# Kernel tuning notes

Measured on AMD Instinct MI355X. Metric: run time of the kernel, lower is better.

## Reference

```python
import jax, jax.numpy as jnp
import numpy as np

B, M, N, DQ, H = 4, 4096, 4096, 256, 64

def setup_inputs() -> dict:
    key = jax.random.key(0)
    k1, k2, k3, k4 = jax.random.split(key, 4)
    x = jax.random.normal(k1, (B, M, DQ), dtype=jnp.float32)
    cond = jax.random.normal(k2, (B, N, DQ), dtype=jnp.float32)
    Wq = jax.random.normal(k3, (DQ, H), dtype=jnp.float32) * (1.0 / np.sqrt(DQ))
    Wkv = jax.random.normal(k4, (DQ, 2 * H), dtype=jnp.float32) * (1.0 / np.sqrt(DQ))
    return {"x": x, "cond": cond, "Wq": Wq, "Wkv": Wkv}

def reference(x, cond, Wq, Wkv):
    h = Wq.shape[1]
    q = jnp.einsum('bmi,ih->bmh', x, Wq)          # [B,M,H]
    kv = jnp.einsum('bni,ih->bnh', cond, Wkv)     # [B,N,2H]
    k, v = jnp.split(kv, 2, axis=-1)              # each [B,N,H]
    qk = jnp.einsum('bmd,bnd->bmn', q, k) / jnp.sqrt(jnp.asarray(h, q.dtype))
    attn = jax.nn.softmax(qk, axis=-1)            # [B,M,N]
    out = jnp.einsum('bmn,bnd->bmd', attn, v)     # [B,M,H]
    return out
```

## Files before the change

kernel.cpp:

```cpp
#include <hip/hip_runtime.h>
#include <hip/hip_bf16.h>
#include <cstdint>


#define BB 4
#define MM 4096
#define NN 4096
#define DQm 256
#define DH 64
#define NSP 8
#define NITER (NN / 64 / NSP)
#define QSCALE 0.18033688011112042f

typedef _Float16 half8 __attribute__((ext_vector_type(8)));
typedef _Float16 half4 __attribute__((ext_vector_type(4)));
typedef float floatx16 __attribute__((ext_vector_type(16)));

static __device__ __forceinline__ unsigned pkrtz(float a, float b) {
    union { __fp16 h __attribute__((ext_vector_type(2))); unsigned u; } cv;
    cv.h = __builtin_amdgcn_cvt_pkrtz(a, b);
    return cv.u;
}

__global__ __launch_bounds__(256) void wtrans_kernel(const float* __restrict__ Wq,
                                                     const float* __restrict__ Wkv,
                                                     _Float16* __restrict__ wt) {
    int cout = blockIdx.x;
    int t = threadIdx.x;
    float v = (cout < 64) ? Wq[t * 64 + cout] * QSCALE : Wkv[t * 128 + (cout - 64)];
    _Float16 hi = (_Float16)v;
    _Float16 lo = (_Float16)(v - (float)hi);
    wt[cout * DQm + t] = hi;
    wt[192 * DQm + cout * DQm + t] = lo;
}

__global__ __launch_bounds__(256) void proj_kernel(const float* __restrict__ x,
                                                   const float* __restrict__ cond,
                                                   const _Float16* __restrict__ wt,
                                                   _Float16* __restrict__ q_h,
                                                   _Float16* __restrict__ k_h,
                                                   _Float16* __restrict__ vt_h) {
    __shared__ __align__(16) _Float16 xh[64][264];
    __shared__ __align__(16) _Float16 xl[64][264];
    const int t = threadIdx.x;
    const bool isq = blockIdx.x < (BB * MM / 64);
    const int blk = isq ? blockIdx.x : blockIdx.x - BB * MM / 64;
    const long row0 = (long)blk * 64;
    const float4* xg = (const float4*)((isq ? x : cond) + row0 * DQm);
#pragma unroll
    for (int it = 0; it < 16; ++it) {
        int fid = t + it * 256;
        int row = fid >> 6, c4 = fid & 63;
        float4 v = xg[fid];
        half4 hh = {(_Float16)v.x, (_Float16)v.y, (_Float16)v.z, (_Float16)v.w};
        half4 hl = {(_Float16)(v.x - (float)hh[0]), (_Float16)(v.y - (float)hh[1]),
                    (_Float16)(v.z - (float)hh[2]), (_Float16)(v.w - (float)hh[3])};
        *(half4*)(&xh[row][c4 * 4]) = hh;
        *(half4*)(&xl[row][c4 * 4]) = hl;
    }
    __syncthreads();
    const int lane = t & 63, w = t >> 6, c = lane & 31, h = lane >> 5;
    const _Float16* wlo = wt + 192 * DQm;

    if (isq) {
        const int rt = w & 1, ct = w >> 1;
        floatx16 a1, a2, a3;
#pragma unroll
        for (int i = 0; i < 16; ++i) { a1[i] = 0.f; a2[i] = 0.f; a3[i] = 0.f; }
#pragma unroll
        for (int kt = 0; kt < 16; ++kt) {
            half8 ah = *(const half8*)(&xh[rt * 32 + c][kt * 16 + h * 8]);
            half8 al = *(const half8*)(&xl[rt * 32 + c][kt * 16 + h * 8]);
            half8 bh = *(const half8*)(wt  + (long)(ct * 32 + c) * DQm + kt * 16 + h * 8);
            half8 bl = *(const half8*)(wlo + (long)(ct * 32 + c) * DQm + kt * 16 + h * 8);
            a1 = __builtin_amdgcn_mfma_f32_32x32x16_f16(ah, bh, a1, 0, 0, 0);
            a2 = __builtin_amdgcn_mfma_f32_32x32x16_f16(ah, bl, a2, 0, 0, 0);
            a3 = __builtin_amdgcn_mfma_f32_32x32x16_f16(al, bh, a3, 0, 0, 0);
        }
#pragma unroll
        for (int r = 0; r < 16; ++r) {
            int m = (r & 3) + 8 * (r >> 2) + 4 * h;
            q_h[(row0 + rt * 32 + m) * DH + ct * 32 + c] = (_Float16)(a1[r] + a2[r] + a3[r]);
        }
    } else {
        const int rt = w & 1, ctp = w >> 1;
        floatx16 a1[2], a2[2], a3[2];
#pragma unroll
        for (int i = 0; i < 16; ++i) {
            a1[0][i] = 0.f; a2[0][i] = 0.f; a3[0][i] = 0.f;
            a1[1][i] = 0.f; a2[1][i] = 0.f; a3[1][i] = 0.f;
        }
#pragma unroll
        for (int kt = 0; kt < 16; ++kt) {
            half8 ah = *(const half8*)(&xh[rt * 32 + c][kt * 16 + h * 8]);
            half8 al = *(const half8*)(&xl[rt * 32 + c][kt * 16 + h * 8]);
#pragma unroll
            for (int i = 0; i < 2; ++i) {
                long wrow = 64 + (ctp * 2 + i) * 32 + c;
                half8 bh = *(const half8*)(wt  + wrow * DQm + kt * 16 + h * 8);
                half8 bl = *(const half8*)(wlo + wrow * DQm + kt * 16 + h * 8);
                a1[i] = __builtin_amdgcn_mfma_f32_32x32x16_f16(ah, bh, a1[i], 0, 0, 0);
                a2[i] = __builtin_amdgcn_mfma_f32_32x32x16_f16(ah, bl, a2[i], 0, 0, 0);
                a3[i] = __builtin_amdgcn_mfma_f32_32x32x16_f16(al, bh, a3[i], 0, 0, 0);
            }
        }
#pragma unroll
        for (int i = 0; i < 2; ++i) {
            int cout = (ctp * 2 + i) * 32 + c;
            if (cout < 64) {
#pragma unroll
                for (int r = 0; r < 16; ++r) {
                    int m = (r & 3) + 8 * (r >> 2) + 4 * h;
                    k_h[(row0 + rt * 32 + m) * DH + cout] =
                        (_Float16)(a1[i][r] + a2[i][r] + a3[i][r]);
                }
            } else {
                int d = cout - 64;
                long bb = row0 >> 12;
#pragma unroll
                for (int s2 = 0; s2 < 4; ++s2) {
                    long n = row0 + rt * 32 + 8 * s2 + 4 * h;
                    half4 hv;
#pragma unroll
                    for (int j = 0; j < 4; ++j)
                        hv[j] = (_Float16)(a1[i][s2 * 4 + j] + a2[i][s2 * 4 + j] +
                                           a3[i][s2 * 4 + j]);
                    *(half4*)(vt_h + (bb * DH + d) * NN + (n & 4095)) = hv;
                }
            }
        }
    }
}

__global__ __launch_bounds__(256, 4) void fa_kernel(const _Float16* __restrict__ q_h,
                                                    const _Float16* __restrict__ k_h,
                                                    const _Float16* __restrict__ vt_h,
                                                    float* __restrict__ Opart,
                                                    float2* __restrict__ ml) {
    __shared__ __align__(16) _Float16 k_lds[64][72];
    __shared__ __align__(16) _Float16 vt_lds[64][72];

    const int t = threadIdx.x;
    const int w = t >> 6;
    const int lane = t & 63;
    const int c = lane & 31;
    const int h = lane >> 5;

    const int bid = blockIdx.x;
    const int sp = bid >> 7;
    const int b  = (bid >> 5) & 3;
    const int mt = bid & 31;
    const int mbase = mt * 128 + w * 32;
    const long qrow = (long)b * MM + mbase + c;

    half8 qf[4];
#pragma unroll
    for (int kt = 0; kt < 4; ++kt)
        qf[kt] = *(const half8*)(q_h + qrow * DH + kt * 16 + h * 8);

    floatx16 Oc0, Oc1;
#pragma unroll
    for (int i = 0; i < 16; ++i) { Oc0[i] = 0.f; Oc1[i] = 0.f; }
    float m_run = -INFINITY, l_run = 0.f;

#pragma unroll 1
    for (int nt = sp * NITER; nt < sp * NITER + NITER; ++nt) {
        const int n0 = nt * 64;
        __syncthreads();
        {
            const uint4* kg = (const uint4*)(k_h + ((long)b * NN + n0) * DH);
#pragma unroll
            for (int it = 0; it < 2; ++it) {
                int cid = t + it * 256;
                int r = cid >> 3, q = cid & 7;
                *(uint4*)(&k_lds[r][q * 8]) = kg[cid];
                *(uint4*)(&vt_lds[r][q * 8]) =
                    *(const uint4*)(vt_h + ((long)b * DH + r) * NN + n0 + q * 8);
            }
        }
        __syncthreads();

        floatx16 Sc[2];
#pragma unroll
        for (int a = 0; a < 2; ++a) {
            floatx16 acc;
#pragma unroll
            for (int i = 0; i < 16; ++i) acc[i] = 0.f;
#pragma unroll
            for (int kt = 0; kt < 4; ++kt) {
                half8 af = *(const half8*)(&k_lds[a * 32 + c][kt * 16 + h * 8]);
                acc = __builtin_amdgcn_mfma_f32_32x32x16_f16(af, qf[kt], acc, 0, 0, 0);
            }
            Sc[a] = acc;
        }

        float tmax = -INFINITY;
#pragma unroll
        for (int a = 0; a < 2; ++a)
#pragma unroll
            for (int r = 0; r < 16; ++r) tmax = fmaxf(tmax, Sc[a][r]);
        tmax = fmaxf(tmax, __shfl_xor(tmax, 32, 64));
        if (__any(tmax > m_run + 8.0f)) {
            float m_new = fmaxf(m_run, tmax);
            float alpha = exp2f(m_run - m_new);
            l_run *= alpha;
#pragma unroll
            for (int i = 0; i < 16; ++i) { Oc0[i] *= alpha; Oc1[i] *= alpha; }
            m_run = m_new;
        }
        float tsum = 0.f;
#pragma unroll
        for (int a = 0; a < 2; ++a)
#pragma unroll
            for (int r = 0; r < 16; ++r) {
                float p = exp2f(Sc[a][r] - m_run);
                Sc[a][r] = p;
                tsum += p;
            }
        tsum += __shfl_xor(tsum, 32, 64);
        l_run += tsum;

#pragma unroll
        for (int a = 0; a < 2; ++a) {
            uint2 pk0 = {pkrtz(Sc[a][0],  Sc[a][1]),  pkrtz(Sc[a][2],  Sc[a][3])};
            uint2 pk1 = {pkrtz(Sc[a][4],  Sc[a][5]),  pkrtz(Sc[a][6],  Sc[a][7])};
            uint2 pk2 = {pkrtz(Sc[a][8],  Sc[a][9]),  pkrtz(Sc[a][10], Sc[a][11])};
            uint2 pk3 = {pkrtz(Sc[a][12], Sc[a][13]), pkrtz(Sc[a][14], Sc[a][15])};
            union { uint4 u; half8 f; } f0, f1;
#if __has_builtin(__builtin_amdgcn_permlane32_swap)
            {
                auto r0 = __builtin_amdgcn_permlane32_swap(pk0.x, pk1.x, false, false);
                auto r1 = __builtin_amdgcn_permlane32_swap(pk0.y, pk1.y, false, false);
                auto r2 = __builtin_amdgcn_permlane32_swap(pk2.x, pk3.x, false, false);
                auto r3 = __builtin_amdgcn_permlane32_swap(pk2.y, pk3.y, false, false);
                f0.u.x = r0[0]; f0.u.z = r0[1];
                f0.u.y = r1[0]; f0.u.w = r1[1];
                f1.u.x = r2[0]; f1.u.z = r2[1];
                f1.u.y = r3[0]; f1.u.w = r3[1];
            }
#else
            {
                uint2 s0, s1, ex0, ex1;
                s0.x = h ? pk0.x : pk1.x;  s0.y = h ? pk0.y : pk1.y;
                s1.x = h ? pk2.x : pk3.x;  s1.y = h ? pk2.y : pk3.y;
                ex0.x = __shfl_xor((int)s0.x, 32, 64);
                ex0.y = __shfl_xor((int)s0.y, 32, 64);
                ex1.x = __shfl_xor((int)s1.x, 32, 64);
                ex1.y = __shfl_xor((int)s1.y, 32, 64);
                f0.u.x = h ? ex0.x : pk0.x;  f0.u.y = h ? ex0.y : pk0.y;
                f0.u.z = h ? pk1.x : ex0.x;  f0.u.w = h ? pk1.y : ex0.y;
                f1.u.x = h ? ex1.x : pk2.x;  f1.u.y = h ? ex1.y : pk2.y;
                f1.u.z = h ? pk3.x : ex1.x;  f1.u.w = h ? pk3.y : ex1.y;
            }
#endif
#pragma unroll
            for (int bq = 0; bq < 2; ++bq) {
                int kt = 2 * a + bq;
                half8 pf = bq ? f1.f : f0.f;
                half8 vf0 = *(const half8*)(&vt_lds[c][kt * 16 + h * 8]);
                half8 vf1 = *(const half8*)(&vt_lds[32 + c][kt * 16 + h * 8]);
                Oc0 = __builtin_amdgcn_mfma_f32_32x32x16_f16(vf0, pf, Oc0, 0, 0, 0);
                Oc1 = __builtin_amdgcn_mfma_f32_32x32x16_f16(vf1, pf, Oc1, 0, 0, 0);
            }
        }
    }

    const long obase = ((long)sp * BB * MM + (long)b * MM + mbase + c) * DH;
#pragma unroll
    for (int dt = 0; dt < 2; ++dt) {
        const floatx16& O = dt ? Oc1 : Oc0;
#pragma unroll
        for (int s2 = 0; s2 < 4; ++s2) {
            float4 v;
            v.x = O[s2 * 4 + 0]; v.y = O[s2 * 4 + 1];
            v.z = O[s2 * 4 + 2]; v.w = O[s2 * 4 + 3];
            *(float4*)(Opart + obase + dt * 32 + s2 * 8 + h * 4) = v;
        }
    }
    if (h == 0)
        ml[((long)sp * BB + b) * MM + mbase + c] = make_float2(m_run, l_run);
}

__global__ __launch_bounds__(256) void merge_kernel(const float* __restrict__ Opart,
                                                    const float2* __restrict__ ml,
                                                    float* __restrict__ out) {
    const long gid = (long)blockIdx.x * 256 + threadIdx.x;
    const long row = gid >> 6;
    float2 p[NSP];
    float mmax = -INFINITY;
#pragma unroll
    for (int i = 0; i < NSP; ++i) {
        p[i] = ml[(long)i * BB * MM + row];
        mmax = fmaxf(mmax, p[i].x);
    }
    float denom = 0.f, o = 0.f;
#pragma unroll
    for (int i = 0; i < NSP; ++i) {
        float ai = exp2f(p[i].x - mmax);
        denom += ai * p[i].y;
        o += ai * Opart[(long)i * BB * MM * DH + gid];
    }
    out[gid] = o / denom;
}

extern "C" void kernel_launch(void* const* d_in, const int* in_sizes, int n_in,
                              void* d_out, int out_size, void* d_ws, size_t ws_size,
                              hipStream_t stream) {
    const float* x    = (const float*)d_in[0];
    const float* cond = (const float*)d_in[1];
    const float* Wq   = (const float*)d_in[2];
    const float* Wkv  = (const float*)d_in[3];
    float* out = (float*)d_out;

    char* ws = (char*)d_ws;
    _Float16* wt   = (_Float16*)(ws);
    _Float16* q_h  = (_Float16*)(ws + 196608);
    _Float16* k_h  = (_Float16*)(ws + 196608 + 2097152);
    _Float16* vt_h = (_Float16*)(ws + 196608 + 2 * 2097152);
    float*    Op   = (float*)(ws + 196608 + 3 * 2097152);
    float2*   mlp  = (float2*)(ws + 196608 + 3 * 2097152 + (size_t)NSP * 4194304);

    wtrans_kernel<<<192, 256, 0, stream>>>(Wq, Wkv, wt);
    proj_kernel<<<BB * (MM + NN) / 64, 256, 0, stream>>>(x, cond, wt, q_h, k_h, vt_h);
    fa_kernel<<<NSP * BB * 32, 256, 0, stream>>>(q_h, k_h, vt_h, Op, mlp);
    merge_kernel<<<BB * MM * DH / 256, 256, 0, stream>>>(Op, mlp, out);
}
```

Baseline: 134.9 us.

## Add MFMA priority hints, tree reductions, fixed m_run init, vectorized merge

Wraps the QK and PV MFMA blocks in s_setprio so waves issuing matrix ops get scheduling priority over softmax ALU work. The serial row-max and row-sum chains become tree reductions to shorten dependency latency. m_run starts at 8.0 instead of -inf, which avoids a guaranteed rescale on the first tile but relies on the lazy-rescale threshold keeping exp2 values bounded. The merge kernel now handles four outputs per thread with float4 loads and stores, using a quarter as many threads and one reciprocal.

```diff
diff --git a/kernel.cpp b/kernel.cpp
--- a/kernel.cpp
+++ b/kernel.cpp
@@ -161,7 +161,7 @@
     floatx16 Oc0, Oc1;
 #pragma unroll
     for (int i = 0; i < 16; ++i) { Oc0[i] = 0.f; Oc1[i] = 0.f; }
-    float m_run = -INFINITY, l_run = 0.f;
+    float m_run = 8.0f, l_run = 0.f;
 
 #pragma unroll 1
     for (int nt = sp * NITER; nt < sp * NITER + NITER; ++nt) {
@@ -181,6 +181,7 @@
         __syncthreads();
 
         floatx16 Sc[2];
+        __builtin_amdgcn_s_setprio(1);
 #pragma unroll
         for (int a = 0; a < 2; ++a) {
             floatx16 acc;
@@ -193,12 +194,16 @@
             }
             Sc[a] = acc;
         }
-
-        float tmax = -INFINITY;
-#pragma unroll
-        for (int a = 0; a < 2; ++a)
-#pragma unroll
-            for (int r = 0; r < 16; ++r) tmax = fmaxf(tmax, Sc[a][r]);
+        __builtin_amdgcn_s_setprio(0);
+
+        float t8v[8];
+#pragma unroll
+        for (int i = 0; i < 8; ++i)
+            t8v[i] = fmaxf(fmaxf(Sc[0][2 * i], Sc[0][2 * i + 1]),
+                           fmaxf(Sc[1][2 * i], Sc[1][2 * i + 1]));
+        float ta = fmaxf(fmaxf(t8v[0], t8v[1]), t8v[2]);
+        float tb = fmaxf(fmaxf(t8v[3], t8v[4]), t8v[5]);
+        float tmax = fmaxf(fmaxf(ta, tb), fmaxf(t8v[6], t8v[7]));
         tmax = fmaxf(tmax, __shfl_xor(tmax, 32, 64));
         if (__any(tmax > m_run + 8.0f)) {
             float m_new = fmaxf(m_run, tmax);
@@ -208,17 +213,24 @@
             for (int i = 0; i < 16; ++i) { Oc0[i] *= alpha; Oc1[i] *= alpha; }
             m_run = m_new;
         }
-        float tsum = 0.f;
 #pragma unroll
         for (int a = 0; a < 2; ++a)
 #pragma unroll
-            for (int r = 0; r < 16; ++r) {
-                float p = exp2f(Sc[a][r] - m_run);
-                Sc[a][r] = p;
-                tsum += p;
-            }
-        tsum += __shfl_xor(tsum, 32, 64);
-        l_run += tsum;
+            for (int r = 0; r < 16; ++r) Sc[a][r] = exp2f(Sc[a][r] - m_run);
+
+        {
+            float ts[16];
+#pragma unroll
+            for (int i = 0; i < 16; ++i) ts[i] = Sc[0][i] + Sc[1][i];
+#pragma unroll
+            for (int i = 0; i < 8; ++i) ts[i] += ts[i + 8];
+#pragma unroll
+            for (int i = 0; i < 4; ++i) ts[i] += ts[i + 4];
+            ts[0] += ts[2]; ts[1] += ts[3];
+            float tsum = ts[0] + ts[1];
+            tsum += __shfl_xor(tsum, 32, 64);
+            l_run += tsum;
+        }
 
 #pragma unroll
         for (int a = 0; a < 2; ++a) {
@@ -229,14 +241,14 @@
             union { uint4 u; half8 f; } f0, f1;
 #if __has_builtin(__builtin_amdgcn_permlane32_swap)
             {
-                auto r0 = __builtin_amdgcn_permlane32_swap(pk0.x, pk1.x, false, false);
-                auto r1 = __builtin_amdgcn_permlane32_swap(pk0.y, pk1.y, false, false);
-                auto r2 = __builtin_amdgcn_permlane32_swap(pk2.x, pk3.x, false, false);
-                auto r3 = __builtin_amdgcn_permlane32_swap(pk2.y, pk3.y, false, false);
-                f0.u.x = r0[0]; f0.u.z = r0[1];
-                f0.u.y = r1[0]; f0.u.w = r1[1];
-                f1.u.x = r2[0]; f1.u.z = r2[1];
-                f1.u.y = r3[0]; f1.u.w = r3[1];
+                auto r0s = __builtin_amdgcn_permlane32_swap(pk0.x, pk1.x, false, false);
+                auto r1s = __builtin_amdgcn_permlane32_swap(pk0.y, pk1.y, false, false);
+                auto r2s = __builtin_amdgcn_permlane32_swap(pk2.x, pk3.x, false, false);
+                auto r3s = __builtin_amdgcn_permlane32_swap(pk2.y, pk3.y, false, false);
+                f0.u.x = r0s[0]; f0.u.z = r0s[1];
+                f0.u.y = r1s[0]; f0.u.w = r1s[1];
+                f1.u.x = r2s[0]; f1.u.z = r2s[1];
+                f1.u.y = r3s[0]; f1.u.w = r3s[1];
             }
 #else
             {
@@ -253,6 +265,7 @@
                 f1.u.z = h ? pk3.x : ex1.x;  f1.u.w = h ? pk3.y : ex1.y;
             }
 #endif
+            __builtin_amdgcn_s_setprio(1);
 #pragma unroll
             for (int bq = 0; bq < 2; ++bq) {
                 int kt = 2 * a + bq;
@@ -262,6 +275,7 @@
                 Oc0 = __builtin_amdgcn_mfma_f32_32x32x16_f16(vf0, pf, Oc0, 0, 0, 0);
                 Oc1 = __builtin_amdgcn_mfma_f32_32x32x16_f16(vf1, pf, Oc1, 0, 0, 0);
             }
+            __builtin_amdgcn_s_setprio(0);
         }
     }
 
@@ -284,8 +298,8 @@
 __global__ __launch_bounds__(256) void merge_kernel(const float* __restrict__ Opart,
                                                     const float2* __restrict__ ml,
                                                     float* __restrict__ out) {
-    const long gid = (long)blockIdx.x * 256 + threadIdx.x;
-    const long row = gid >> 6;
+    const long g4 = (long)blockIdx.x * 256 + threadIdx.x;
+    const long row = g4 >> 4;
     float2 p[NSP];
     float mmax = -INFINITY;
 #pragma unroll
@@ -293,14 +307,19 @@
         p[i] = ml[(long)i * BB * MM + row];
         mmax = fmaxf(mmax, p[i].x);
     }
-    float denom = 0.f, o = 0.f;
+    float denom = 0.f;
+    float4 o = make_float4(0.f, 0.f, 0.f, 0.f);
+    const float4* Op4 = (const float4*)Opart;
 #pragma unroll
     for (int i = 0; i < NSP; ++i) {
         float ai = exp2f(p[i].x - mmax);
         denom += ai * p[i].y;
-        o += ai * Opart[(long)i * BB * MM * DH + gid];
-    }
-    out[gid] = o / denom;
+        float4 v = Op4[(long)i * (BB * MM * DH / 4) + g4];
+        o.x += ai * v.x; o.y += ai * v.y; o.z += ai * v.z; o.w += ai * v.w;
+    }
+    float inv = 1.0f / denom;
+    o.x *= inv; o.y *= inv; o.z *= inv; o.w *= inv;
+    ((float4*)out)[g4] = o;
 }
 
 extern "C" void kernel_launch(void* const* d_in, const int* in_sizes, int n_in,
@@ -323,5 +342,5 @@
     wtrans_kernel<<<192, 256, 0, stream>>>(Wq, Wkv, wt);
     proj_kernel<<<BB * (MM + NN) / 64, 256, 0, stream>>>(x, cond, wt, q_h, k_h, vt_h);
     fa_kernel<<<NSP * BB * 32, 256, 0, stream>>>(q_h, k_h, vt_h, Op, mlp);
-    merge_kernel<<<BB * MM * DH / 256, 256, 0, stream>>>(Op, mlp, out);
-}
+    merge_kernel<<<BB * MM * DH / 4 / 256, 256, 0, stream>>>(Op, mlp, out);
+}
```

After: 133.2 us. About the same (-1.2%).
